# Kernel tuning notes

Hardware: AMD Instinct MI355X
Metric: run time of the kernel (lower is better)

The kernel has to match this reference:

```python
import jax, jax.numpy as jnp
import numpy as np

N_HEADS = 16

def setup_inputs() -> dict:
    key = jax.random.key(0)
    ks = jax.random.split(key, 4)
    B, T, C = 2, 2048, 1024
    scale = 0.02
    return {
        "x": jax.random.normal(ks[0], (B, T, C), dtype=jnp.float32),
        "w_qkv": jax.random.normal(ks[1], (C, 3 * C), dtype=jnp.float32) * scale,
        "b_qkv": jnp.zeros((3 * C,), dtype=jnp.float32),
        "w_out": jax.random.normal(ks[2], (C, C), dtype=jnp.float32) * scale,
        "b_out": jnp.zeros((C,), dtype=jnp.float32),
    }

def reference(x, w_qkv, b_qkv, w_out, b_out):
    B, T, C = x.shape
    H = N_HEADS
    hd = C // H
    qkv = x @ w_qkv + b_qkv                      # [B,T,3C]
    q, k, v = jnp.split(qkv, 3, axis=-1)
    # [B,H,T,hd]
    q = q.reshape(B, T, H, hd).transpose(0, 2, 1, 3)
    k = k.reshape(B, T, H, hd).transpose(0, 2, 1, 3)
    v = v.reshape(B, T, H, hd).transpose(0, 2, 1, 3)
    att = jnp.einsum('bhqd,bhkd->bhqk', q, k) / jnp.sqrt(jnp.float32(hd))
    causal = jnp.tril(jnp.ones((T, T), dtype=bool))
    att = jnp.where(causal, att, -jnp.inf)
    att = jax.nn.softmax(att, axis=-1)
    # dropout is identity in eval mode (p effectively 0 for reference)
    y = jnp.einsum('bhqk,bhkd->bhqd', att, v)
    y = y.transpose(0, 2, 1, 3).reshape(B, T, C)
    return y @ w_out + b_out
```

## Files before the change

kernel.cpp:

```cpp
#include <hip/hip_runtime.h>
#include <hip/hip_bf16.h>

#define DEVI __device__ __forceinline__

typedef __attribute__((ext_vector_type(8))) short bf16x8_t;
typedef __attribute__((ext_vector_type(4))) float f32x4_t;
typedef __attribute__((ext_vector_type(4))) short s16x4_t;
typedef __attribute__((ext_vector_type(2))) unsigned int u32x2_t;

#define QSCALE 0.18033688011112043f
#define EXP2F(x) __builtin_amdgcn_exp2f(x)

static DEVI unsigned short f2b_bits(float f) {
    unsigned int u = __float_as_uint(f);
    unsigned int r = (u + 0x7fffu + ((u >> 16) & 1u)) >> 16;
    return (unsigned short)r;
}

static DEVI unsigned int cvtpk_bf16(float lo, float hi) {
    unsigned int r;
    asm("v_cvt_pk_bf16_f32 %0, %1, %2" : "=v"(r) : "v"(lo), "v"(hi));
    return r;
}

static DEVI void gload16(const short* g, short* l) {
    __builtin_amdgcn_global_load_lds((const __attribute__((address_space(1))) void*)g,
                                     (__attribute__((address_space(3))) void*)l, 16, 0, 0);
}

#define MEMFENCE asm volatile("" ::: "memory")

__global__ __launch_bounds__(256) void prep_k(const float* __restrict__ x, short* __restrict__ xb,
                                              const float* __restrict__ wqkv, short* __restrict__ wqkvT,
                                              const float* __restrict__ wout, short* __restrict__ woutT) {
    const int bid = blockIdx.x;
    const int tid = threadIdx.x;
    if (bid < 4096) {
        const long i = ((long)bid * 256 + tid) * 4;
        const float4 v = *(const float4*)(x + i);
        s16x4_t o;
        o[0] = (short)f2b_bits(v.x); o[1] = (short)f2b_bits(v.y);
        o[2] = (short)f2b_bits(v.z); o[3] = (short)f2b_bits(v.w);
        *(s16x4_t*)(xb + i) = o;
        return;
    }
    __shared__ float tile[32][33];
    const float* w; short* wT; int K, N, bx, by;
    if (bid < 4096 + 3072) {
        const int rel = bid - 4096;
        w = wqkv; wT = wqkvT; K = 1024; N = 3072; bx = rel % 96; by = rel / 96;
    } else {
        const int rel = bid - 7168;
        w = wout; wT = woutT; K = 1024; N = 1024; bx = rel & 31; by = rel >> 5;
    }
    const int n0 = bx * 32, k0 = by * 32;
    const int tx = tid & 31, ty = tid >> 5;
#pragma unroll
    for (int i = 0; i < 4; ++i)
        tile[ty + 8 * i][tx] = w[(long)(k0 + ty + 8 * i) * N + n0 + tx];
    __syncthreads();
#pragma unroll
    for (int i = 0; i < 4; ++i)
        wT[(long)(n0 + ty + 8 * i) * K + k0 + tx] = (short)f2b_bits(tile[tx][ty + 8 * i]);
}

template<int MODE, int NF>
__global__ __launch_bounds__(256, 3) void gemm_bt(const short* __restrict__ A,
                                                  const short* __restrict__ Bt,
                                                  const float* __restrict__ bias,
                                                  void* __restrict__ Cv,
                                                  short* __restrict__ vtp,
                                                  int M, int N, int K) {
    __shared__ __align__(16) short lsA[2][128 * 32];
    __shared__ __align__(16) short lsB[2][32 * NF * 32];
    const int tid = threadIdx.x;
    const int lane = tid & 63;
    const int w = tid >> 6;
    const int wr = w >> 1, wc = w & 1;
    const int l15 = lane & 15, lg = lane >> 4;
    const long m0 = (long)blockIdx.y * 128;
    const long n0 = (long)blockIdx.x * (32 * NF);

    f32x4_t acc[4][NF] = {};

    const int srow = tid >> 2;
    const int scol = (tid & 3) * 8;
    const short* gA = A + (m0 + srow) * (long)K + scol;
    const short* gB = Bt + (n0 + srow) * (long)K + scol;

    auto STAGE = [&](int kt, int bi) {
        gload16(gA + kt,                &lsA[bi][tid * 8]);
        gload16(gA + kt + (long)64 * K, &lsA[bi][tid * 8 + 2048]);
        gload16(gB + kt,                &lsB[bi][tid * 8]);
        if (NF == 4) gload16(gB + kt + (long)64 * K, &lsB[bi][tid * 8 + 2048]);
    };

    const int nt = K >> 5;
    STAGE(0, 0);
    int buf = 0;

    for (int i = 0; i < nt; ++i) {
        if (i + 1 < nt) {
            STAGE((i + 1) << 5, buf ^ 1);
            if (NF == 4) asm volatile("s_waitcnt vmcnt(4)" ::: "memory");
            else         asm volatile("s_waitcnt vmcnt(3)" ::: "memory");
        } else {
            asm volatile("s_waitcnt vmcnt(0)" ::: "memory");
        }
        __builtin_amdgcn_s_barrier();
        MEMFENCE;
        bf16x8_t af[4], bfr[NF];
#pragma unroll
        for (int m = 0; m < 4; ++m)
            af[m] = *(const bf16x8_t*)&lsA[buf][(wr * 64 + m * 16 + l15) * 32 + lg * 8];
#pragma unroll
        for (int n = 0; n < NF; ++n)
            bfr[n] = *(const bf16x8_t*)&lsB[buf][(wc * NF * 16 + n * 16 + l15) * 32 + lg * 8];
#pragma unroll
        for (int m = 0; m < 4; ++m)
#pragma unroll
            for (int n = 0; n < NF; ++n)
                acc[m][n] = __builtin_amdgcn_mfma_f32_16x16x32_bf16(af[m], bfr[n], acc[m][n], 0, 0, 0);
        MEMFENCE;
        __builtin_amdgcn_s_barrier();
        buf ^= 1;
    }

#pragma unroll
    for (int n = 0; n < NF; ++n) {
        const int col = (int)n0 + wc * NF * 16 + n * 16 + l15;
        const float bv = bias[col];
        if (MODE == 1) {
#pragma unroll
            for (int m = 0; m < 4; ++m) {
                const long row = m0 + wr * 64 + m * 16 + lg * 4;
#pragma unroll
                for (int j = 0; j < 4; ++j)
                    ((float*)Cv)[(row + j) * N + col] = acc[m][n][j] + bv;
            }
        } else if (col < 2048) {
            const float sc = (col < 1024) ? QSCALE : 1.0f;
#pragma unroll
            for (int m = 0; m < 4; ++m) {
                const long row = m0 + wr * 64 + m * 16 + lg * 4;
#pragma unroll
                for (int j = 0; j < 4; ++j)
                    ((short*)Cv)[(row + j) * N + col] = (short)f2b_bits((acc[m][n][j] + bv) * sc);
            }
        } else {
            const int hc = col - 2048;
            const int hh = hc >> 6, dd = hc & 63;
#pragma unroll
            for (int m = 0; m < 4; ++m) {
                const long row = m0 + wr * 64 + m * 16 + lg * 4;
                const int bb = (int)(row >> 11), tt = (int)(row & 2047);
                s16x4_t pk;
#pragma unroll
                for (int j = 0; j < 4; ++j) pk[j] = (short)f2b_bits(acc[m][n][j] + bv);
                *(s16x4_t*)&vtp[((long)(bb * 16 + hh) * 64 + dd) * 2048 + tt] = pk;
            }
        }
    }
}

__global__ __launch_bounds__(256, 4) void attn_fwd(const short* __restrict__ qkv,
                                                   const short* __restrict__ vt,
                                                   short* __restrict__ y) {
    __shared__ __align__(16) short lsK[2][64 * 64];
    __shared__ __align__(16) short lsV[2][64 * 64];
    __shared__ __align__(16) short lsP[4 * 16 * 64];
    const int bid = blockIdx.x;
    const int bh = bid & 31;
    const int t = bid >> 5;
    const int qi = (t < 16) ? t : 47 - t;
    const int b = bh >> 4, h = bh & 15;
    const int tid = threadIdx.x, w = tid >> 6, lane = tid & 63;
    const int l15 = lane & 15, lg = lane >> 4;
    const int lg4 = lg * 4;
    const int swz = (l15 & 7) << 4;

    const long qrow = (long)qi * 64 + w * 16 + l15;
    const bf16x8_t qf0 = *(const bf16x8_t*)&qkv[((long)b * 2048 + qrow) * 3072 + h * 64 + lg * 8];
    const bf16x8_t qf1 = *(const bf16x8_t*)&qkv[((long)b * 2048 + qrow) * 3072 + h * 64 + 32 + lg * 8];

    const int srow = tid >> 3;
    const int scolb = (tid & 7) * 16;
    const int sc = (scolb ^ ((srow & 7) << 4)) >> 1;
    const short* gK = qkv + ((long)b * 2048 + srow) * 3072 + 1024 + h * 64 + sc;
    const short* gV = vt + ((long)bh * 64 + srow) * 2048 + sc;

    auto STAGE = [&](int jt, int bufi) {
        const short* k0 = gK + (long)jt * 64 * 3072;
        const short* v0 = gV + (long)jt * 64;
        gload16(k0,             &lsK[bufi][tid * 8]);
        gload16(k0 + 32 * 3072, &lsK[bufi][tid * 8 + 2048]);
        gload16(v0,             &lsV[bufi][tid * 8]);
        gload16(v0 + 32 * 2048, &lsV[bufi][tid * 8 + 2048]);
    };

    float mrow = -3e38f, lrow = 0.f;
    f32x4_t oacc[4] = {};

    STAGE(0, 0);
    int buf = 0;

    for (int j = 0; j <= qi; ++j) {
        if (j < qi) {
            STAGE(j + 1, buf ^ 1);
            asm volatile("s_waitcnt vmcnt(4)" ::: "memory");
        } else {
            asm volatile("s_waitcnt vmcnt(0)" ::: "memory");
        }
        __builtin_amdgcn_s_barrier();
        MEMFENCE;

        const bool diag = (j == qi);
        const char* Kb = (const char*)lsK[buf];
        const char* Vb = (const char*)lsV[buf];

        f32x4_t s[4] = {};
        const int nlim = diag ? (w + 1) : 4;
        __builtin_amdgcn_s_setprio(1);
#pragma unroll
        for (int kq = 0; kq < 2; ++kq) {
            const bf16x8_t qf = kq ? qf1 : qf0;
#pragma unroll
            for (int n = 0; n < 4; ++n) {
                if (n < nlim) {
                    bf16x8_t kf = *(const bf16x8_t*)(Kb + (n * 16 + l15) * 128 + ((kq * 64 + lg * 16) ^ swz));
                    s[n] = __builtin_amdgcn_mfma_f32_16x16x32_bf16(kf, qf, s[n], 0, 0, 0);
                }
            }
        }
        __builtin_amdgcn_s_setprio(0);

        float p[4][4];
#pragma unroll
        for (int n = 0; n < 4; ++n)
#pragma unroll
            for (int r = 0; r < 4; ++r) p[n][r] = s[n][r];

        if (diag) {
            const int ql = w * 16 + l15 - lg4;
#pragma unroll
            for (int n = 0; n < 4; ++n)
#pragma unroll
                for (int r = 0; r < 4; ++r)
                    if (n * 16 + r > ql) p[n][r] = -3e38f;
        }

        float pm = -3e38f;
#pragma unroll
        for (int n = 0; n < 4; ++n)
            pm = fmaxf(pm, fmaxf(fmaxf(p[n][0], p[n][1]), fmaxf(p[n][2], p[n][3])));
        pm = fmaxf(pm, __shfl_xor(pm, 16));
        pm = fmaxf(pm, __shfl_xor(pm, 32));

        if (!__all(pm <= mrow + 8.f)) {
            const float mnew = fmaxf(mrow, pm);
            const float al = EXP2F(mrow - mnew);
            mrow = mnew;
            lrow *= al;
            float ar[4];
#pragma unroll
            for (int r = 0; r < 4; ++r) ar[r] = __shfl(al, lg4 + r);
#pragma unroll
            for (int n = 0; n < 4; ++n)
#pragma unroll
                for (int r = 0; r < 4; ++r) oacc[n][r] *= ar[r];
        }

        float lsum = 0.f;
        char* Pb = (char*)lsP + w * 2048 + l15 * 128;
#pragma unroll
        for (int n = 0; n < 4; ++n) {
#pragma unroll
            for (int r = 0; r < 4; ++r) {
                p[n][r] = EXP2F(p[n][r] - mrow);
                lsum += p[n][r];
            }
            u32x2_t dw;
            dw[0] = cvtpk_bf16(p[n][0], p[n][1]);
            dw[1] = cvtpk_bf16(p[n][2], p[n][3]);
            *(u32x2_t*)(Pb + ((n * 32 + lg * 8) ^ swz)) = dw;
        }
        lsum += __shfl_xor(lsum, 16);
        lsum += __shfl_xor(lsum, 32);
        lrow += lsum;

        asm volatile("s_waitcnt lgkmcnt(0)" ::: "memory");

        __builtin_amdgcn_s_setprio(1);
#pragma unroll
        for (int kk = 0; kk < 2; ++kk) {
            if (!(diag && kk * 32 > w * 16 + 15)) {
                bf16x8_t pf = *(const bf16x8_t*)(Pb + ((kk * 64 + lg * 16) ^ swz));
#pragma unroll
                for (int n = 0; n < 4; ++n) {
                    bf16x8_t vf = *(const bf16x8_t*)(Vb + (n * 16 + l15) * 128 + ((kk * 64 + lg * 16) ^ swz));
                    oacc[n] = __builtin_amdgcn_mfma_f32_16x16x32_bf16(pf, vf, oacc[n], 0, 0, 0);
                }
            }
        }
        __builtin_amdgcn_s_setprio(0);
        MEMFENCE;
        __builtin_amdgcn_s_barrier();
        buf ^= 1;
    }

    float lr[4];
#pragma unroll
    for (int r = 0; r < 4; ++r) lr[r] = 1.0f / __shfl(lrow, lg4 + r);
#pragma unroll
    for (int n = 0; n < 4; ++n)
#pragma unroll
        for (int r = 0; r < 4; ++r) {
            const float ov = oacc[n][r] * lr[r];
            y[((long)b * 2048 + qi * 64 + w * 16 + lg4 + r) * 1024 + h * 64 + n * 16 + l15] =
                (short)f2b_bits(ov);
        }
}

extern "C" void kernel_launch(void* const* d_in, const int* in_sizes, int n_in,
                              void* d_out, int out_size, void* d_ws, size_t ws_size,
                              hipStream_t stream) {
    const float* x     = (const float*)d_in[0];
    const float* w_qkv = (const float*)d_in[1];
    const float* b_qkv = (const float*)d_in[2];
    const float* w_out = (const float*)d_in[3];
    const float* b_out = (const float*)d_in[4];

    char* ws = (char*)d_ws;
    size_t off = 0;
    short* xb    = (short*)(ws + off); off += (size_t)4096 * 1024 * 2;
    short* wqkvT = (short*)(ws + off); off += (size_t)3072 * 1024 * 2;
    short* woutT = (short*)(ws + off); off += (size_t)1024 * 1024 * 2;
    short* qkvb  = (short*)(ws + off); off += (size_t)4096 * 3072 * 2;
    short* vt    = (short*)(ws + off); off += (size_t)32 * 64 * 2048 * 2;
    short* yatt  = (short*)(ws + off); off += (size_t)4096 * 1024 * 2;

    prep_k<<<8192, 256, 0, stream>>>(x, xb, w_qkv, wqkvT, w_out, woutT);
    gemm_bt<0, 4><<<dim3(24, 32), 256, 0, stream>>>(xb, wqkvT, b_qkv, (void*)qkvb, vt, 4096, 3072, 1024);
    attn_fwd<<<1024, 256, 0, stream>>>(qkvb, vt, yatt);
    gemm_bt<1, 2><<<dim3(16, 32), 256, 0, stream>>>(yatt, woutT, b_out, d_out, nullptr, 4096, 1024, 1024);
}
```

Before: 179.4 us.

## Process paired causal query tiles per block to share K/V loads

Each attention block now handles two query tiles (qA and 31-qA) of the same head. Every K/V tile staged into shared memory feeds both tiles' QK and PV MFMAs, which halves K/V global traffic and balances causal work across blocks. The grid shrinks from 1024 to 512 blocks and launch bounds drop to 2 blocks per CU, since register use (two accumulator sets) and LDS (doubled P buffer) grow. Fewer, heavier blocks lower occupancy and give the scheduler less latency hiding.

```diff
diff --git a/kernel.cpp b/kernel.cpp
--- a/kernel.cpp
+++ b/kernel.cpp
@@ -163,25 +163,31 @@
     }
 }
 
-__global__ __launch_bounds__(256, 4) void attn_fwd(const short* __restrict__ qkv,
+__global__ __launch_bounds__(256, 2) void attn_fwd(const short* __restrict__ qkv,
                                                    const short* __restrict__ vt,
                                                    short* __restrict__ y) {
     __shared__ __align__(16) short lsK[2][64 * 64];
     __shared__ __align__(16) short lsV[2][64 * 64];
-    __shared__ __align__(16) short lsP[4 * 16 * 64];
+    __shared__ __align__(16) short lsP[2 * 4 * 16 * 64];
     const int bid = blockIdx.x;
     const int bh = bid & 31;
     const int t = bid >> 5;
-    const int qi = (t < 16) ? t : 47 - t;
+    const int pair = (t < 8) ? t : 23 - t;
+    const int qA = pair, qB = 31 - pair;
     const int b = bh >> 4, h = bh & 15;
     const int tid = threadIdx.x, w = tid >> 6, lane = tid & 63;
     const int l15 = lane & 15, lg = lane >> 4;
     const int lg4 = lg * 4;
     const int swz = (l15 & 7) << 4;
 
-    const long qrow = (long)qi * 64 + w * 16 + l15;
-    const bf16x8_t qf0 = *(const bf16x8_t*)&qkv[((long)b * 2048 + qrow) * 3072 + h * 64 + lg * 8];
-    const bf16x8_t qf1 = *(const bf16x8_t*)&qkv[((long)b * 2048 + qrow) * 3072 + h * 64 + 32 + lg * 8];
+    const long qrowA = (long)qA * 64 + w * 16 + l15;
+    const long qrowB = (long)qB * 64 + w * 16 + l15;
+    bf16x8_t qfA[2], qfB[2];
+#pragma unroll
+    for (int kq = 0; kq < 2; ++kq) {
+        qfA[kq] = *(const bf16x8_t*)&qkv[((long)b * 2048 + qrowA) * 3072 + h * 64 + kq * 32 + lg * 8];
+        qfB[kq] = *(const bf16x8_t*)&qkv[((long)b * 2048 + qrowB) * 3072 + h * 64 + kq * 32 + lg * 8];
+    }
 
     const int srow = tid >> 3;
     const int scolb = (tid & 7) * 16;
@@ -198,14 +204,17 @@
         gload16(v0 + 32 * 2048, &lsV[bufi][tid * 8 + 2048]);
     };
 
-    float mrow = -3e38f, lrow = 0.f;
-    f32x4_t oacc[4] = {};
+    float mA = -3e38f, lA = 0.f, mB = -3e38f, lB = 0.f;
+    f32x4_t oA[4] = {}, oB[4] = {};
 
     STAGE(0, 0);
     int buf = 0;
 
-    for (int j = 0; j <= qi; ++j) {
-        if (j < qi) {
+    char* PbA = (char*)lsP + w * 2048 + l15 * 128;
+    char* PbB = PbA + 8192;
+
+    for (int j = 0; j <= qB; ++j) {
+        if (j < qB) {
             STAGE(j + 1, buf ^ 1);
             asm volatile("s_waitcnt vmcnt(4)" ::: "memory");
         } else {
@@ -214,91 +223,142 @@
         __builtin_amdgcn_s_barrier();
         MEMFENCE;
 
-        const bool diag = (j == qi);
+        const bool actA = (j <= qA);
+        const bool diagA = (j == qA), diagB = (j == qB);
         const char* Kb = (const char*)lsK[buf];
         const char* Vb = (const char*)lsV[buf];
-
-        f32x4_t s[4] = {};
-        const int nlim = diag ? (w + 1) : 4;
+        const int nlimB = diagB ? (w + 1) : 4;
+        const int nlimA = diagA ? (w + 1) : 4;
+
+        f32x4_t sA[4] = {}, sB[4] = {};
         __builtin_amdgcn_s_setprio(1);
 #pragma unroll
         for (int kq = 0; kq < 2; ++kq) {
-            const bf16x8_t qf = kq ? qf1 : qf0;
 #pragma unroll
             for (int n = 0; n < 4; ++n) {
-                if (n < nlim) {
+                if (n < nlimB) {
                     bf16x8_t kf = *(const bf16x8_t*)(Kb + (n * 16 + l15) * 128 + ((kq * 64 + lg * 16) ^ swz));
-                    s[n] = __builtin_amdgcn_mfma_f32_16x16x32_bf16(kf, qf, s[n], 0, 0, 0);
+                    sB[n] = __builtin_amdgcn_mfma_f32_16x16x32_bf16(kf, qfB[kq], sB[n], 0, 0, 0);
+                    if (actA && n < nlimA)
+                        sA[n] = __builtin_amdgcn_mfma_f32_16x16x32_bf16(kf, qfA[kq], sA[n], 0, 0, 0);
                 }
             }
         }
         __builtin_amdgcn_s_setprio(0);
 
-        float p[4][4];
+        float pB[4][4], pA[4][4];
 #pragma unroll
         for (int n = 0; n < 4; ++n)
 #pragma unroll
-            for (int r = 0; r < 4; ++r) p[n][r] = s[n][r];
-
-        if (diag) {
+            for (int r = 0; r < 4; ++r) pB[n][r] = sB[n][r];
+        if (diagB) {
             const int ql = w * 16 + l15 - lg4;
 #pragma unroll
             for (int n = 0; n < 4; ++n)
 #pragma unroll
                 for (int r = 0; r < 4; ++r)
-                    if (n * 16 + r > ql) p[n][r] = -3e38f;
-        }
-
-        float pm = -3e38f;
+                    if (n * 16 + r > ql) pB[n][r] = -3e38f;
+        }
+        float pmB = -3e38f;
 #pragma unroll
         for (int n = 0; n < 4; ++n)
-            pm = fmaxf(pm, fmaxf(fmaxf(p[n][0], p[n][1]), fmaxf(p[n][2], p[n][3])));
-        pm = fmaxf(pm, __shfl_xor(pm, 16));
-        pm = fmaxf(pm, __shfl_xor(pm, 32));
-
-        if (!__all(pm <= mrow + 8.f)) {
-            const float mnew = fmaxf(mrow, pm);
-            const float al = EXP2F(mrow - mnew);
-            mrow = mnew;
-            lrow *= al;
+            pmB = fmaxf(pmB, fmaxf(fmaxf(pB[n][0], pB[n][1]), fmaxf(pB[n][2], pB[n][3])));
+        pmB = fmaxf(pmB, __shfl_xor(pmB, 16));
+        pmB = fmaxf(pmB, __shfl_xor(pmB, 32));
+
+        if (actA) {
+#pragma unroll
+            for (int n = 0; n < 4; ++n)
+#pragma unroll
+                for (int r = 0; r < 4; ++r) pA[n][r] = sA[n][r];
+            if (diagA) {
+                const int ql = w * 16 + l15 - lg4;
+#pragma unroll
+                for (int n = 0; n < 4; ++n)
+#pragma unroll
+                    for (int r = 0; r < 4; ++r)
+                        if (n * 16 + r > ql) pA[n][r] = -3e38f;
+            }
+            float pmA = -3e38f;
+#pragma unroll
+            for (int n = 0; n < 4; ++n)
+                pmA = fmaxf(pmA, fmaxf(fmaxf(pA[n][0], pA[n][1]), fmaxf(pA[n][2], pA[n][3])));
+            pmA = fmaxf(pmA, __shfl_xor(pmA, 16));
+            pmA = fmaxf(pmA, __shfl_xor(pmA, 32));
+            if (!__all(pmA <= mA + 8.f)) {
+                const float mnew = fmaxf(mA, pmA);
+                const float al = EXP2F(mA - mnew);
+                mA = mnew; lA *= al;
+                float ar[4];
+#pragma unroll
+                for (int r = 0; r < 4; ++r) ar[r] = __shfl(al, lg4 + r);
+#pragma unroll
+                for (int n = 0; n < 4; ++n)
+#pragma unroll
+                    for (int r = 0; r < 4; ++r) oA[n][r] *= ar[r];
+            }
+            float lsA_ = 0.f;
+#pragma unroll
+            for (int n = 0; n < 4; ++n) {
+#pragma unroll
+                for (int r = 0; r < 4; ++r) {
+                    pA[n][r] = EXP2F(pA[n][r] - mA);
+                    lsA_ += pA[n][r];
+                }
+                u32x2_t dw;
+                dw[0] = cvtpk_bf16(pA[n][0], pA[n][1]);
+                dw[1] = cvtpk_bf16(pA[n][2], pA[n][3]);
+                *(u32x2_t*)(PbA + ((n * 32 + lg * 8) ^ swz)) = dw;
+            }
+            lsA_ += __shfl_xor(lsA_, 16);
+            lsA_ += __shfl_xor(lsA_, 32);
+            lA += lsA_;
+        }
+
+        if (!__all(pmB <= mB + 8.f)) {
+            const float mnew = fmaxf(mB, pmB);
+            const float al = EXP2F(mB - mnew);
+            mB = mnew; lB *= al;
             float ar[4];
 #pragma unroll
             for (int r = 0; r < 4; ++r) ar[r] = __shfl(al, lg4 + r);
 #pragma unroll
             for (int n = 0; n < 4; ++n)
 #pragma unroll
-                for (int r = 0; r < 4; ++r) oacc[n][r] *= ar[r];
-        }
-
-        float lsum = 0.f;
-        char* Pb = (char*)lsP + w * 2048 + l15 * 128;
+                for (int r = 0; r < 4; ++r) oB[n][r] *= ar[r];
+        }
+        float lsB_ = 0.f;
 #pragma unroll
         for (int n = 0; n < 4; ++n) {
 #pragma unroll
             for (int r = 0; r < 4; ++r) {
-                p[n][r] = EXP2F(p[n][r] - mrow);
-                lsum += p[n][r];
+                pB[n][r] = EXP2F(pB[n][r] - mB);
+                lsB_ += pB[n][r];
             }
             u32x2_t dw;
-            dw[0] = cvtpk_bf16(p[n][0], p[n][1]);
-            dw[1] = cvtpk_bf16(p[n][2], p[n][3]);
-            *(u32x2_t*)(Pb + ((n * 32 + lg * 8) ^ swz)) = dw;
-        }
-        lsum += __shfl_xor(lsum, 16);
-        lsum += __shfl_xor(lsum, 32);
-        lrow += lsum;
+            dw[0] = cvtpk_bf16(pB[n][0], pB[n][1]);
+            dw[1] = cvtpk_bf16(pB[n][2], pB[n][3]);
+            *(u32x2_t*)(PbB + ((n * 32 + lg * 8) ^ swz)) = dw;
+        }
+        lsB_ += __shfl_xor(lsB_, 16);
+        lsB_ += __shfl_xor(lsB_, 32);
+        lB += lsB_;
 
         asm volatile("s_waitcnt lgkmcnt(0)" ::: "memory");
 
         __builtin_amdgcn_s_setprio(1);
 #pragma unroll
         for (int kk = 0; kk < 2; ++kk) {
-            if (!(diag && kk * 32 > w * 16 + 15)) {
-                bf16x8_t pf = *(const bf16x8_t*)(Pb + ((kk * 64 + lg * 16) ^ swz));
+            const bool kkB = !(diagB && kk * 32 > w * 16 + 15);
+            const bool kkA = actA && !(diagA && kk * 32 > w * 16 + 15);
+            if (kkA || kkB) {
+                bf16x8_t pfB = *(const bf16x8_t*)(PbB + ((kk * 64 + lg * 16) ^ swz));
+                bf16x8_t pfA = *(const bf16x8_t*)(PbA + ((kk * 64 + lg * 16) ^ swz));
 #pragma unroll
                 for (int n = 0; n < 4; ++n) {
                     bf16x8_t vf = *(const bf16x8_t*)(Vb + (n * 16 + l15) * 128 + ((kk * 64 + lg * 16) ^ swz));
-                    oacc[n] = __builtin_amdgcn_mfma_f32_16x16x32_bf16(pf, vf, oacc[n], 0, 0, 0);
+                    if (kkB) oB[n] = __builtin_amdgcn_mfma_f32_16x16x32_bf16(pfB, vf, oB[n], 0, 0, 0);
+                    if (kkA) oA[n] = __builtin_amdgcn_mfma_f32_16x16x32_bf16(pfA, vf, oA[n], 0, 0, 0);
                 }
             }
         }
@@ -308,16 +368,20 @@
         buf ^= 1;
     }
 
-    float lr[4];
-#pragma unroll
-    for (int r = 0; r < 4; ++r) lr[r] = 1.0f / __shfl(lrow, lg4 + r);
+    float lrA[4], lrB[4];
+#pragma unroll
+    for (int r = 0; r < 4; ++r) {
+        lrA[r] = 1.0f / __shfl(lA, lg4 + r);
+        lrB[r] = 1.0f / __shfl(lB, lg4 + r);
+    }
 #pragma unroll
     for (int n = 0; n < 4; ++n)
 #pragma unroll
         for (int r = 0; r < 4; ++r) {
-            const float ov = oacc[n][r] * lr[r];
-            y[((long)b * 2048 + qi * 64 + w * 16 + lg4 + r) * 1024 + h * 64 + n * 16 + l15] =
-                (short)f2b_bits(ov);
+            y[((long)b * 2048 + qA * 64 + w * 16 + lg4 + r) * 1024 + h * 64 + n * 16 + l15] =
+                (short)f2b_bits(oA[n][r] * lrA[r]);
+            y[((long)b * 2048 + qB * 64 + w * 16 + lg4 + r) * 1024 + h * 64 + n * 16 + l15] =
+                (short)f2b_bits(oB[n][r] * lrB[r]);
         }
 }
 
@@ -341,6 +405,6 @@
 
     prep_k<<<8192, 256, 0, stream>>>(x, xb, w_qkv, wqkvT, w_out, woutT);
     gemm_bt<0, 4><<<dim3(24, 32), 256, 0, stream>>>(xb, wqkvT, b_qkv, (void*)qkvb, vt, 4096, 3072, 1024);
-    attn_fwd<<<1024, 256, 0, stream>>>(qkvb, vt, yatt);
+    attn_fwd<<<512, 256, 0, stream>>>(qkvb, vt, yatt);
     gemm_bt<1, 2><<<dim3(16, 32), 256, 0, stream>>>(yatt, woutT, b_out, d_out, nullptr, 4096, 1024, 1024);
 }
```

New measurement: 200.9 us. +12.0%, slower.
